# Kernel optimization log

Hardware: AMD Instinct MI355X
Metric: run time of the kernel (lower is better)

The kernel has to match this reference:

```python
import jax, jax.numpy as jnp
import numpy as np

N = 50000   # num_nodes
E = 400000  # random edges (avg degree 8)


def setup_inputs() -> dict:
    key = jax.random.key(0)
    ks = jax.random.split(key, 12)

    def w(k, shape):
        # xavier-ish scaling
        return (jax.random.normal(k, shape, jnp.float32)
                / jnp.sqrt(jnp.float32(shape[0])))

    return {
        "node_emb": jax.random.normal(ks[0], (N, 128), jnp.float32) * 0.05,
        "edge_index": jax.random.randint(ks[1], (2, E), 0, N, dtype=jnp.int32),
        "W1": w(ks[2], (128, 512)), "b1": jnp.zeros((512,), jnp.float32),
        "W2": w(ks[3], (512, 128)), "b2": jnp.zeros((128,), jnp.float32),
        "Wres": w(ks[4], (512, 128)), "bres": jnp.zeros((128,), jnp.float32),
        "Wfc1": w(ks[5], (128, 256)), "bfc1": jnp.zeros((256,), jnp.float32),
        "Wfc2": w(ks[6], (256, 1)), "bfc2": jnp.zeros((1,), jnp.float32),
    }


def reference(node_emb, edge_index, W1, b1, W2, b2, Wres, bres,
              Wfc1, bfc1, Wfc2, bfc2):
    n = node_emb.shape[0]
    loops = jnp.arange(n, dtype=edge_index.dtype)
    # explicit add_self_loops in forward + GCNConv's internal gcn_norm self
    # loops => each node gets TWO self loops (faithful to the torch code).
    src = jnp.concatenate([edge_index[0], loops, loops])
    dst = jnp.concatenate([edge_index[1], loops, loops])

    deg = jax.ops.segment_sum(jnp.ones(src.shape, node_emb.dtype), dst,
                              num_segments=n)
    dinv = jnp.where(deg > 0, jax.lax.rsqrt(deg), 0.0)
    norm = dinv[src] * dinv[dst]  # [Etot]

    def gcn(x, W, b):
        h = x @ W                                    # [N, out]
        msg = h[src] * norm[:, None]                 # gather + scale
        agg = jax.ops.segment_sum(msg, dst, num_segments=n)  # scatter-add
        return agg + b

    x1 = jax.nn.relu(gcn(node_emb, W1, b1))   # [N, 512] (dropout = eval/id)
    x2 = jax.nn.relu(gcn(x1, W2, b2))          # [N, 128]
    x = x2 + x1 @ Wres + bres                  # residual projection
    A = jax.nn.relu(x @ Wfc1 + bfc1) @ Wfc2 + bfc2  # [N, 1]
    return (x, A)
```

## Files before the change

kernel.cpp:

```cpp
#include <hip/hip_runtime.h>


typedef unsigned short u16;
typedef short bf16x8 __attribute__((ext_vector_type(8)));
typedef unsigned short us8 __attribute__((ext_vector_type(8)));
typedef float f32x4 __attribute__((ext_vector_type(4)));

static inline int cdiv_ll(long long a, long long b) { return (int)((a + b - 1) / b); }

__device__ inline float bf2f(u16 u) {
    union { unsigned int i; float f; } v; v.i = ((unsigned int)u) << 16; return v.f;
}
__device__ inline u16 f2bf(float x) {
    union { float f; unsigned int i; } v; v.f = x;
    unsigned int r = v.i + 0x7fffu + ((v.i >> 16) & 1u);
    return (u16)(r >> 16);
}


__global__ __launch_bounds__(256) void setup_kernel(const float* __restrict__ emb,
                                                    const float* __restrict__ W1,
                                                    const float* __restrict__ W2,
                                                    const float* __restrict__ Wres,
                                                    const float* __restrict__ Wfc1,
                                                    const float* __restrict__ bfc2,
                                                    u16* __restrict__ embb,
                                                    u16* __restrict__ W1t,
                                                    u16* __restrict__ Wct,
                                                    u16* __restrict__ Wfc1t,
                                                    int* __restrict__ cnt,
                                                    float* __restrict__ Aout,
                                                    int N) {
    long long r = (long long)blockIdx.x * 256 + threadIdx.x;
    const long long nf2b = (long long)N * 32;
    if (r < nf2b) {
        float4 v = ((const float4*)emb)[r];
        uint2 o;
        o.x = (unsigned)f2bf(v.x) | ((unsigned)f2bf(v.y) << 16);
        o.y = (unsigned)f2bf(v.z) | ((unsigned)f2bf(v.w) << 16);
        ((uint2*)embb)[r] = o;
        return;
    }
    r -= nf2b;
    if (r < 512 * 128) {
        int n = (int)(r / 128), k = (int)(r % 128);
        W1t[r] = f2bf(W1[(size_t)k * 512 + n]);
        return;
    }
    r -= 512 * 128;
    if (r < 256 * 512) {
        int n = (int)(r / 512), k = (int)(r % 512);
        float v = (n < 128) ? W2[(size_t)k * 128 + n] : Wres[(size_t)k * 128 + (n - 128)];
        Wct[r] = f2bf(v);
        return;
    }
    r -= 256 * 512;
    if (r < 256 * 128) {
        int n = (int)(r / 128), k = (int)(r % 128);
        Wfc1t[r] = f2bf(Wfc1[(size_t)k * 256 + n]);
        return;
    }
    r -= 256 * 128;
    if (r < N) { cnt[(int)r] = 0; return; }
    r -= N;
    if (r < N) Aout[(int)r] = bfc2[0];
}


__global__ __launch_bounds__(256) void hist_kernel(const int* __restrict__ dst,
                                                   int* __restrict__ cnt, int E) {
    int e = blockIdx.x * 256 + threadIdx.x;
    if (e < E) atomicAdd(&cnt[dst[e]], 1);
}

__global__ __launch_bounds__(256) void scanA_kernel(const int* __restrict__ cnt,
                                                    int* __restrict__ excl,
                                                    int* __restrict__ bsum, int N) {
    __shared__ int tmp[256];
    int i = blockIdx.x * 256 + threadIdx.x;
    int v = (i < N) ? cnt[i] : 0;
    tmp[threadIdx.x] = v;
    __syncthreads();
    for (int o = 1; o < 256; o <<= 1) {
        int t = (threadIdx.x >= (unsigned)o) ? tmp[threadIdx.x - o] : 0;
        __syncthreads();
        tmp[threadIdx.x] += t;
        __syncthreads();
    }
    if (i < N) excl[i] = tmp[threadIdx.x] - v;
    if (threadIdx.x == 255) bsum[blockIdx.x] = tmp[255];
}

__global__ __launch_bounds__(256) void scanC2_kernel(const int* __restrict__ excl,
                                                     const int* __restrict__ bsum,
                                                     const int* __restrict__ cnt,
                                                     int* __restrict__ rowptr,
                                                     int* __restrict__ cursor,
                                                     float* __restrict__ dinv,
                                                     int N, int E) {
    __shared__ int tmp[256];
    int t = threadIdx.x;
    tmp[t] = (t < (int)blockIdx.x) ? bsum[t] : 0;
    __syncthreads();
    for (int o = 128; o; o >>= 1) {
        if (t < o) tmp[t] += tmp[t + o];
        __syncthreads();
    }
    int pre = tmp[0];
    int i = blockIdx.x * 256 + t;
    if (i < N) {
        int r = excl[i] + pre;
        rowptr[i] = r;
        cursor[i] = r;
        dinv[i] = rsqrtf((float)cnt[i] + 2.0f);
    }
    if (i == 0) rowptr[N] = E;
}

__global__ __launch_bounds__(256) void fill_kernel(const int* __restrict__ src,
                                                   const int* __restrict__ dst,
                                                   const float* __restrict__ dinv,
                                                   int* __restrict__ cursor,
                                                   int* __restrict__ csr_src,
                                                   float* __restrict__ csr_w, int E) {
    int e = blockIdx.x * 256 + threadIdx.x;
    if (e >= E) return;
    int s = src[e], d = dst[e];
    int idx = atomicAdd(&cursor[d], 1);
    csr_src[idx] = s;
    csr_w[idx] = dinv[s] * dinv[d];
}


#define AGG_EDGE(SR, WR)                                                       \
    {                                                                          \
        unsigned int vv = hp[(size_t)(SR) * 64 + lane];                        \
        ax = fmaf(bf2f((u16)vv), (WR), ax);                                    \
        ay = fmaf(bf2f((u16)(vv >> 16)), (WR), ay);                            \
    }

__device__ inline void agg_row(const unsigned int* __restrict__ hp,
                               const int* __restrict__ rowptr,
                               const int* __restrict__ csr_src,
                               const float* __restrict__ csr_w,
                               const float* __restrict__ dinv,
                               int wid, int lane, float& ax, float& ay) {
    float dv = dinv[wid];
    unsigned int hv = hp[(size_t)wid * 64 + lane];
    float c0 = 2.0f * dv * dv;
    ax = bf2f((u16)hv) * c0;
    ay = bf2f((u16)(hv >> 16)) * c0;
    int e = rowptr[wid], e1 = rowptr[wid + 1];
    for (; e + 7 < e1; e += 8) {
        int s0 = csr_src[e + 0], s1 = csr_src[e + 1], s2 = csr_src[e + 2], s3 = csr_src[e + 3];
        int s4 = csr_src[e + 4], s5 = csr_src[e + 5], s6 = csr_src[e + 6], s7 = csr_src[e + 7];
        float w0 = csr_w[e + 0], w1 = csr_w[e + 1], w2 = csr_w[e + 2], w3 = csr_w[e + 3];
        float w4 = csr_w[e + 4], w5 = csr_w[e + 5], w6 = csr_w[e + 6], w7 = csr_w[e + 7];
        AGG_EDGE(s0, w0); AGG_EDGE(s1, w1); AGG_EDGE(s2, w2); AGG_EDGE(s3, w3);
        AGG_EDGE(s4, w4); AGG_EDGE(s5, w5); AGG_EDGE(s6, w6); AGG_EDGE(s7, w7);
    }
    if (e + 3 < e1) {
        int s0 = csr_src[e + 0], s1 = csr_src[e + 1], s2 = csr_src[e + 2], s3 = csr_src[e + 3];
        float w0 = csr_w[e + 0], w1 = csr_w[e + 1], w2 = csr_w[e + 2], w3 = csr_w[e + 3];
        AGG_EDGE(s0, w0); AGG_EDGE(s1, w1); AGG_EDGE(s2, w2); AGG_EDGE(s3, w3);
        e += 4;
    }
    for (; e < e1; ++e) {
        int s0 = csr_src[e]; float w0 = csr_w[e];
        AGG_EDGE(s0, w0);
    }
}

__global__ __launch_bounds__(256) void aggb_kernel(const u16* __restrict__ hb,
                                                   const int* __restrict__ rowptr,
                                                   const int* __restrict__ csr_src,
                                                   const float* __restrict__ csr_w,
                                                   const float* __restrict__ dinv,
                                                   u16* __restrict__ out, int N) {
    int wid  = (blockIdx.x * blockDim.x + threadIdx.x) >> 6;
    int lane = threadIdx.x & 63;
    if (wid >= N) return;
    float ax, ay;
    agg_row((const unsigned int*)hb, rowptr, csr_src, csr_w, dinv, wid, lane, ax, ay);
    ((unsigned int*)out)[(size_t)wid * 64 + lane] =
        (unsigned)f2bf(ax) | ((unsigned)f2bf(ay) << 16);
}

__global__ __launch_bounds__(256) void aggfin_kernel(const u16* __restrict__ hb,
                                                     const int* __restrict__ rowptr,
                                                     const int* __restrict__ csr_src,
                                                     const float* __restrict__ csr_w,
                                                     const float* __restrict__ dinv,
                                                     const float* __restrict__ b2,
                                                     const float* __restrict__ bres,
                                                     float* __restrict__ xout, int N) {
    int wid  = (blockIdx.x * blockDim.x + threadIdx.x) >> 6;
    int lane = threadIdx.x & 63;
    if (wid >= N) return;
    float ax, ay;
    agg_row((const unsigned int*)hb, rowptr, csr_src, csr_w, dinv, wid, lane, ax, ay);
    float2 bb = ((const float2*)b2)[lane];
    float2 rr = ((const float2*)bres)[lane];
    float2 hres = ((float2*)xout)[(size_t)wid * 64 + lane];
    float ox = fmaxf(ax + bb.x, 0.f) + hres.x + rr.x;
    float oy = fmaxf(ay + bb.y, 0.f) + hres.y + rr.y;
    ((float2*)xout)[(size_t)wid * 64 + lane] = make_float2(ox, oy);
}


__global__ __launch_bounds__(512) void mgemm12(const u16* __restrict__ aggE,
                                               const u16* __restrict__ W1t,
                                               const u16* __restrict__ Wct,
                                               const float* __restrict__ b1,
                                               int M,
                                               u16* __restrict__ h2b,
                                               float* __restrict__ xout) {
    extern __shared__ u16 smem[];
    u16* Ag  = smem;
    u16* Ws  = Ag + 128 * 136;
    u16* X1s = Ws + 256 * 136;
    const int LD = 136;

    const int t = threadIdx.x;
    const int bm = blockIdx.x * 128;
    const int w = t >> 6, lane = t & 63;
    const int wm = w >> 2, wn = w & 3;
    const int l15 = lane & 15, lg = lane >> 4;
    const int srow = t >> 4, scol = (t & 15) * 8;

#pragma unroll
    for (int i = 0; i < 4; ++i) {
        int row = srow + 32 * i;
        us8 v = (us8)(u16)0;
        if (bm + row < M) v = *(const us8*)(aggE + (size_t)(bm + row) * 128 + scol);
        *(us8*)&Ag[row * LD + scol] = v;
    }

    f32x4 acc2[4][4];
#pragma unroll
    for (int i = 0; i < 4; ++i)
#pragma unroll
        for (int j = 0; j < 4; ++j) acc2[i][j] = (f32x4)(0.0f);

    us8 rw1[4], rwc[8];
#pragma unroll
    for (int i = 0; i < 4; ++i)
        rw1[i] = *(const us8*)(W1t + (size_t)(srow + 32 * i) * 128 + scol);

    for (int p = 0; p < 4; ++p) {
        __syncthreads();
#pragma unroll
        for (int i = 0; i < 4; ++i)
            *(us8*)&Ws[(srow + 32 * i) * LD + scol] = rw1[i];
        __syncthreads();

#pragma unroll
        for (int i = 0; i < 8; ++i)
            rwc[i] = *(const us8*)(Wct + (size_t)(srow + 32 * i) * 512 + 128 * p + scol);

        f32x4 acc1[4][2];
#pragma unroll
        for (int i = 0; i < 4; ++i)
#pragma unroll
            for (int j = 0; j < 2; ++j) acc1[i][j] = (f32x4)(0.0f);
#pragma unroll
        for (int ks = 0; ks < 4; ++ks) {
            const int ko = 32 * ks + lg * 8;
            bf16x8 wfr[2], afr[4];
#pragma unroll
            for (int fn = 0; fn < 2; ++fn)
                wfr[fn] = *(const bf16x8*)&Ws[(32 * wn + 16 * fn + l15) * LD + ko];
#pragma unroll
            for (int fm = 0; fm < 4; ++fm)
                afr[fm] = *(const bf16x8*)&Ag[(64 * wm + 16 * fm + l15) * LD + ko];
#pragma unroll
            for (int fm = 0; fm < 4; ++fm)
#pragma unroll
                for (int fn = 0; fn < 2; ++fn)
                    acc1[fm][fn] = __builtin_amdgcn_mfma_f32_16x16x32_bf16(
                        wfr[fn], afr[fm], acc1[fm][fn], 0, 0, 0);
        }
        __syncthreads();

#pragma unroll
        for (int fm = 0; fm < 4; ++fm) {
#pragma unroll
            for (int fn = 0; fn < 2; ++fn) {
                int col1 = 32 * wn + 16 * fn + 4 * lg;
                float4 b4 = *(const float4*)&b1[128 * p + col1];
                f32x4 v = acc1[fm][fn];
                float v0 = fmaxf(v[0] + b4.x, 0.f), v1 = fmaxf(v[1] + b4.y, 0.f);
                float v2 = fmaxf(v[2] + b4.z, 0.f), v3 = fmaxf(v[3] + b4.w, 0.f);
                uint2 o;
                o.x = (unsigned)f2bf(v0) | ((unsigned)f2bf(v1) << 16);
                o.y = (unsigned)f2bf(v2) | ((unsigned)f2bf(v3) << 16);
                *(uint2*)&X1s[(64 * wm + 16 * fm + l15) * LD + col1] = o;
            }
        }
#pragma unroll
        for (int i = 0; i < 8; ++i)
            *(us8*)&Ws[(srow + 32 * i) * LD + scol] = rwc[i];
        if (p < 3) {
#pragma unroll
            for (int i = 0; i < 4; ++i)
                rw1[i] = *(const us8*)(W1t + (size_t)(128 * (p + 1) + srow + 32 * i) * 128 + scol);
        }
        __syncthreads();

#pragma unroll
        for (int ks = 0; ks < 4; ++ks) {
            const int ko = 32 * ks + lg * 8;
            bf16x8 wfr[4], xfr[4];
#pragma unroll
            for (int fn = 0; fn < 4; ++fn)
                wfr[fn] = *(const bf16x8*)&Ws[(64 * wn + 16 * fn + l15) * LD + ko];
#pragma unroll
            for (int fm = 0; fm < 4; ++fm)
                xfr[fm] = *(const bf16x8*)&X1s[(64 * wm + 16 * fm + l15) * LD + ko];
#pragma unroll
            for (int fm = 0; fm < 4; ++fm)
#pragma unroll
                for (int fn = 0; fn < 4; ++fn)
                    acc2[fm][fn] = __builtin_amdgcn_mfma_f32_16x16x32_bf16(
                        wfr[fn], xfr[fm], acc2[fm][fn], 0, 0, 0);
        }
    }

#pragma unroll
    for (int fm = 0; fm < 4; ++fm) {
        const int row = bm + 64 * wm + 16 * fm + l15;
        if (row >= M) continue;
#pragma unroll
        for (int fn = 0; fn < 4; ++fn) {
            const int col = 64 * wn + 16 * fn + 4 * lg;
            f32x4 v = acc2[fm][fn];
            if (col < 128) {
                uint2 o;
                o.x = (unsigned)f2bf(v[0]) | ((unsigned)f2bf(v[1]) << 16);
                o.y = (unsigned)f2bf(v[2]) | ((unsigned)f2bf(v[3]) << 16);
                *(uint2*)(h2b + (size_t)row * 128 + col) = o;
            } else {
                *(float4*)(xout + (size_t)row * 128 + (col - 128)) =
                    make_float4(v[0], v[1], v[2], v[3]);
            }
        }
    }
}


__global__ __launch_bounds__(512) void head_gemm(const float* __restrict__ X,
                                                 const u16* __restrict__ Bt,
                                                 int M,
                                                 const float* __restrict__ bias,
                                                 const float* __restrict__ w2,
                                                 float* __restrict__ Cf) {
    __shared__ u16 As[128][72];
    __shared__ u16 Bs[256][72];
    const int t = threadIdx.x;
    const int bm = blockIdx.x * 128;
    const int w = t >> 6, lane = t & 63;
    const int wm = w >> 2, wn = w & 3;
    const int l15 = lane & 15, lg = lane >> 4;
    const int srow = t >> 3, scol = (t & 7) * 8;
    const int K = 128;

    f32x4 acc[4][4];
#pragma unroll
    for (int i = 0; i < 4; ++i)
#pragma unroll
        for (int j = 0; j < 4; ++j) acc[i][j] = (f32x4)(0.0f);

    for (int kk = 0; kk < K; kk += 64) {
#pragma unroll
        for (int i = 0; i < 2; ++i) {
            int row = srow + 64 * i;
            uint4 o = make_uint4(0u, 0u, 0u, 0u);
            if (bm + row < M) {
                const float* src = X + (size_t)(bm + row) * K + kk + scol;
                float4 a = *(const float4*)src;
                float4 b = *(const float4*)(src + 4);
                o.x = (unsigned)f2bf(a.x) | ((unsigned)f2bf(a.y) << 16);
                o.y = (unsigned)f2bf(a.z) | ((unsigned)f2bf(a.w) << 16);
                o.z = (unsigned)f2bf(b.x) | ((unsigned)f2bf(b.y) << 16);
                o.w = (unsigned)f2bf(b.z) | ((unsigned)f2bf(b.w) << 16);
            }
            *(uint4*)&As[row][scol] = o;
        }
#pragma unroll
        for (int i = 0; i < 4; ++i) {
            int row = srow + 64 * i;
            *(us8*)&Bs[row][scol] =
                *(const us8*)(Bt + (size_t)row * K + kk + scol);
        }
        __syncthreads();
#pragma unroll
        for (int ks = 0; ks < 2; ++ks) {
            const int ko = 32 * ks + lg * 8;
            bf16x8 bfr[4], afr[4];
#pragma unroll
            for (int fn = 0; fn < 4; ++fn)
                bfr[fn] = *(const bf16x8*)&Bs[64 * wn + 16 * fn + l15][ko];
#pragma unroll
            for (int fm = 0; fm < 4; ++fm)
                afr[fm] = *(const bf16x8*)&As[64 * wm + 16 * fm + l15][ko];
#pragma unroll
            for (int fm = 0; fm < 4; ++fm)
#pragma unroll
                for (int fn = 0; fn < 4; ++fn)
                    acc[fm][fn] = __builtin_amdgcn_mfma_f32_16x16x32_bf16(
                        bfr[fn], afr[fm], acc[fm][fn], 0, 0, 0);
        }
        __syncthreads();
    }

    float4 bl4[4], wl4[4];
#pragma unroll
    for (int fn = 0; fn < 4; ++fn) {
        int c = 64 * wn + 16 * fn + 4 * lg;
        bl4[fn] = *(const float4*)&bias[c];
        wl4[fn] = *(const float4*)&w2[c];
    }
#pragma unroll
    for (int fm = 0; fm < 4; ++fm) {
        float p = 0.f;
#pragma unroll
        for (int fn = 0; fn < 4; ++fn) {
            p += fmaxf(acc[fm][fn][0] + bl4[fn].x, 0.f) * wl4[fn].x;
            p += fmaxf(acc[fm][fn][1] + bl4[fn].y, 0.f) * wl4[fn].y;
            p += fmaxf(acc[fm][fn][2] + bl4[fn].z, 0.f) * wl4[fn].z;
            p += fmaxf(acc[fm][fn][3] + bl4[fn].w, 0.f) * wl4[fn].w;
        }
        p += __shfl_xor(p, 16);
        p += __shfl_xor(p, 32);
        int row = bm + 64 * wm + 16 * fm + l15;
        if (lane < 16 && row < M) atomicAdd(&Cf[row], p);
    }
}


extern "C" void kernel_launch(void* const* d_in, const int* in_sizes, int n_in,
                              void* d_out, int out_size, void* d_ws, size_t ws_size,
                              hipStream_t stream) {
    const float* emb  = (const float*)d_in[0];
    const int*   eidx = (const int*)d_in[1];
    const float* W1   = (const float*)d_in[2];
    const float* b1   = (const float*)d_in[3];
    const float* W2   = (const float*)d_in[4];
    const float* b2   = (const float*)d_in[5];
    const float* Wres = (const float*)d_in[6];
    const float* bres = (const float*)d_in[7];
    const float* Wfc1 = (const float*)d_in[8];
    const float* bfc1 = (const float*)d_in[9];
    const float* Wfc2 = (const float*)d_in[10];
    const float* bfc2 = (const float*)d_in[11];

    const int N = in_sizes[0] / 128;
    const int E = in_sizes[1] / 2;
    const int* srcv = eidx;
    const int* dstv = eidx + E;

    float* out  = (float*)d_out;
    float* xout = out;
    float* Aout = out + (size_t)N * 128;

    char* p = (char*)d_ws;
    float* dinv  = (float*)p;            p += (size_t)N * 4;
    float* csr_w = (float*)p;            p += (size_t)E * 4;
    u16*  embb   = (u16*)p;              p += (size_t)N * 128 * 2;
    u16*  aggEb  = (u16*)p;              p += (size_t)N * 128 * 2;
    u16*  h2b    = (u16*)p;              p += (size_t)N * 128 * 2;
    u16*  W1t    = (u16*)p;              p += (size_t)512 * 128 * 2;
    u16*  Wct    = (u16*)p;              p += (size_t)256 * 512 * 2;
    u16*  Wfc1t  = (u16*)p;              p += (size_t)256 * 128 * 2;
    int*  cnt     = (int*)p;             p += (size_t)N * 4;
    int*  excl    = (int*)p;             p += (size_t)N * 4;
    int*  rowptr  = (int*)p;             p += (size_t)(N + 1) * 4;
    int*  cursor  = (int*)p;             p += (size_t)N * 4;
    int*  bsum    = (int*)p;             p += 256 * 4;
    int*  csr_src = (int*)p;             p += (size_t)E * 4;

    const int T  = 256;
    const int nb = cdiv_ll(N, 256);

    const long long setup_work = (long long)N * 32 + 512 * 128 + 256 * 512
                               + 256 * 128 + (long long)N + (long long)N;
    setup_kernel<<<cdiv_ll(setup_work, T), T, 0, stream>>>(
        emb, W1, W2, Wres, Wfc1, bfc2, embb, W1t, Wct, Wfc1t, cnt, Aout, N);

    hist_kernel<<<cdiv_ll(E, T), T, 0, stream>>>(dstv, cnt, E);
    scanA_kernel<<<nb, T, 0, stream>>>(cnt, excl, bsum, N);
    scanC2_kernel<<<nb, T, 0, stream>>>(excl, bsum, cnt, rowptr, cursor, dinv, N, E);
    fill_kernel<<<cdiv_ll(E, T), T, 0, stream>>>(srcv, dstv, dinv, cursor, csr_src, csr_w, E);

    aggb_kernel<<<cdiv_ll((long long)N * 64, T), T, 0, stream>>>(
        embb, rowptr, csr_src, csr_w, dinv, aggEb, N);

    const size_t lds12 = (size_t)(128 * 136 + 256 * 136 + 128 * 136) * sizeof(u16);
    mgemm12<<<cdiv_ll(N, 128), 512, lds12, stream>>>(
        aggEb, W1t, Wct, b1, N, h2b, xout);

    aggfin_kernel<<<cdiv_ll((long long)N * 64, T), T, 0, stream>>>(
        h2b, rowptr, csr_src, csr_w, dinv, b2, bres, xout, N);

    head_gemm<<<cdiv_ll(N, 128), 512, 0, stream>>>(
        xout, Wfc1t, N, bfc1, Wfc2, Aout);
}
```

Before: 175.0 us.

## Split wavefront into four edge groups with 16-byte gathers in aggregation

The two sparse aggregation kernels are merged into one templated kernel. Each wavefront now splits its 64 lanes into four groups of 16. Each group processes every fourth edge and each lane gathers 8 bf16 values (16 bytes) per edge instead of 2. The partial sums are combined with cross-lane shuffles, and a single group writes the result. This is meant to put more independent row gathers in flight per wavefront and to use wider loads, at the cost of extra shuffle reductions and idle lanes in the epilogue.

```diff
diff --git a/kernel.cpp b/kernel.cpp
--- a/kernel.cpp
+++ b/kernel.cpp
@@ -15,6 +15,9 @@
     union { float f; unsigned int i; } v; v.f = x;
     unsigned int r = v.i + 0x7fffu + ((v.i >> 16) & 1u);
     return (u16)(r >> 16);
+}
+__device__ inline unsigned pk2(float a, float b) {
+    return (unsigned)f2bf(a) | ((unsigned)f2bf(b) << 16);
 }
 
 
@@ -36,8 +39,8 @@
     if (r < nf2b) {
         float4 v = ((const float4*)emb)[r];
         uint2 o;
-        o.x = (unsigned)f2bf(v.x) | ((unsigned)f2bf(v.y) << 16);
-        o.y = (unsigned)f2bf(v.z) | ((unsigned)f2bf(v.w) << 16);
+        o.x = pk2(v.x, v.y);
+        o.y = pk2(v.z, v.w);
         ((uint2*)embb)[r] = o;
         return;
     }
@@ -132,79 +135,95 @@
 }
 
 
-#define AGG_EDGE(SR, WR)                                                       \
+#define FMA8(VV, W)                                                            \
     {                                                                          \
-        unsigned int vv = hp[(size_t)(SR) * 64 + lane];                        \
-        ax = fmaf(bf2f((u16)vv), (WR), ax);                                    \
-        ay = fmaf(bf2f((u16)(vv >> 16)), (WR), ay);                            \
-    }
-
-__device__ inline void agg_row(const unsigned int* __restrict__ hp,
-                               const int* __restrict__ rowptr,
-                               const int* __restrict__ csr_src,
-                               const float* __restrict__ csr_w,
-                               const float* __restrict__ dinv,
-                               int wid, int lane, float& ax, float& ay) {
-    float dv = dinv[wid];
-    unsigned int hv = hp[(size_t)wid * 64 + lane];
-    float c0 = 2.0f * dv * dv;
-    ax = bf2f((u16)hv) * c0;
-    ay = bf2f((u16)(hv >> 16)) * c0;
-    int e = rowptr[wid], e1 = rowptr[wid + 1];
-    for (; e + 7 < e1; e += 8) {
-        int s0 = csr_src[e + 0], s1 = csr_src[e + 1], s2 = csr_src[e + 2], s3 = csr_src[e + 3];
-        int s4 = csr_src[e + 4], s5 = csr_src[e + 5], s6 = csr_src[e + 6], s7 = csr_src[e + 7];
-        float w0 = csr_w[e + 0], w1 = csr_w[e + 1], w2 = csr_w[e + 2], w3 = csr_w[e + 3];
-        float w4 = csr_w[e + 4], w5 = csr_w[e + 5], w6 = csr_w[e + 6], w7 = csr_w[e + 7];
-        AGG_EDGE(s0, w0); AGG_EDGE(s1, w1); AGG_EDGE(s2, w2); AGG_EDGE(s3, w3);
-        AGG_EDGE(s4, w4); AGG_EDGE(s5, w5); AGG_EDGE(s6, w6); AGG_EDGE(s7, w7);
-    }
-    if (e + 3 < e1) {
-        int s0 = csr_src[e + 0], s1 = csr_src[e + 1], s2 = csr_src[e + 2], s3 = csr_src[e + 3];
-        float w0 = csr_w[e + 0], w1 = csr_w[e + 1], w2 = csr_w[e + 2], w3 = csr_w[e + 3];
-        AGG_EDGE(s0, w0); AGG_EDGE(s1, w1); AGG_EDGE(s2, w2); AGG_EDGE(s3, w3);
-        e += 4;
-    }
-    for (; e < e1; ++e) {
-        int s0 = csr_src[e]; float w0 = csr_w[e];
-        AGG_EDGE(s0, w0);
-    }
-}
-
-__global__ __launch_bounds__(256) void aggb_kernel(const u16* __restrict__ hb,
+        acc0 = fmaf(bf2f((u16)(VV).x), (W), acc0);                             \
+        acc1 = fmaf(bf2f((u16)((VV).x >> 16)), (W), acc1);                     \
+        acc2 = fmaf(bf2f((u16)(VV).y), (W), acc2);                             \
+        acc3 = fmaf(bf2f((u16)((VV).y >> 16)), (W), acc3);                     \
+        acc4 = fmaf(bf2f((u16)(VV).z), (W), acc4);                             \
+        acc5 = fmaf(bf2f((u16)((VV).z >> 16)), (W), acc5);                     \
+        acc6 = fmaf(bf2f((u16)(VV).w), (W), acc6);                             \
+        acc7 = fmaf(bf2f((u16)((VV).w >> 16)), (W), acc7);                     \
+    }
+
+template <int FINAL>
+__global__ __launch_bounds__(256) void aggq_kernel(const u16* __restrict__ hb,
                                                    const int* __restrict__ rowptr,
                                                    const int* __restrict__ csr_src,
                                                    const float* __restrict__ csr_w,
                                                    const float* __restrict__ dinv,
-                                                   u16* __restrict__ out, int N) {
+                                                   const float* __restrict__ b2,
+                                                   const float* __restrict__ bres,
+                                                   float* __restrict__ xout,
+                                                   u16* __restrict__ outb, int N) {
     int wid  = (blockIdx.x * blockDim.x + threadIdx.x) >> 6;
     int lane = threadIdx.x & 63;
+    int g = lane >> 4, l = lane & 15;
     if (wid >= N) return;
-    float ax, ay;
-    agg_row((const unsigned int*)hb, rowptr, csr_src, csr_w, dinv, wid, lane, ax, ay);
-    ((unsigned int*)out)[(size_t)wid * 64 + lane] =
-        (unsigned)f2bf(ax) | ((unsigned)f2bf(ay) << 16);
-}
-
-__global__ __launch_bounds__(256) void aggfin_kernel(const u16* __restrict__ hb,
-                                                     const int* __restrict__ rowptr,
-                                                     const int* __restrict__ csr_src,
-                                                     const float* __restrict__ csr_w,
-                                                     const float* __restrict__ dinv,
-                                                     const float* __restrict__ b2,
-                                                     const float* __restrict__ bres,
-                                                     float* __restrict__ xout, int N) {
-    int wid  = (blockIdx.x * blockDim.x + threadIdx.x) >> 6;
-    int lane = threadIdx.x & 63;
-    if (wid >= N) return;
-    float ax, ay;
-    agg_row((const unsigned int*)hb, rowptr, csr_src, csr_w, dinv, wid, lane, ax, ay);
-    float2 bb = ((const float2*)b2)[lane];
-    float2 rr = ((const float2*)bres)[lane];
-    float2 hres = ((float2*)xout)[(size_t)wid * 64 + lane];
-    float ox = fmaxf(ax + bb.x, 0.f) + hres.x + rr.x;
-    float oy = fmaxf(ay + bb.y, 0.f) + hres.y + rr.y;
-    ((float2*)xout)[(size_t)wid * 64 + lane] = make_float2(ox, oy);
+    const uint4* hp4 = (const uint4*)hb;
+
+    float acc0 = 0.f, acc1 = 0.f, acc2 = 0.f, acc3 = 0.f;
+    float acc4 = 0.f, acc5 = 0.f, acc6 = 0.f, acc7 = 0.f;
+    float dv = dinv[wid];
+    if (g == 0) {
+        uint4 hv = hp4[(size_t)wid * 16 + l];
+        float c0 = 2.0f * dv * dv;
+        FMA8(hv, c0);
+    }
+
+    int e  = rowptr[wid] + g;
+    int e1 = rowptr[wid + 1];
+    for (; e + 4 < e1; e += 8) {
+        int   s0 = csr_src[e],     s1 = csr_src[e + 4];
+        float w0 = csr_w[e],       w1 = csr_w[e + 4];
+        uint4 v0 = hp4[(size_t)s0 * 16 + l];
+        uint4 v1 = hp4[(size_t)s1 * 16 + l];
+        FMA8(v0, w0);
+        FMA8(v1, w1);
+    }
+    if (e < e1) {
+        int s0 = csr_src[e]; float w0 = csr_w[e];
+        uint4 v0 = hp4[(size_t)s0 * 16 + l];
+        FMA8(v0, w0);
+    }
+
+    acc0 += __shfl_xor(acc0, 16); acc0 += __shfl_xor(acc0, 32);
+    acc1 += __shfl_xor(acc1, 16); acc1 += __shfl_xor(acc1, 32);
+    acc2 += __shfl_xor(acc2, 16); acc2 += __shfl_xor(acc2, 32);
+    acc3 += __shfl_xor(acc3, 16); acc3 += __shfl_xor(acc3, 32);
+    acc4 += __shfl_xor(acc4, 16); acc4 += __shfl_xor(acc4, 32);
+    acc5 += __shfl_xor(acc5, 16); acc5 += __shfl_xor(acc5, 32);
+    acc6 += __shfl_xor(acc6, 16); acc6 += __shfl_xor(acc6, 32);
+    acc7 += __shfl_xor(acc7, 16); acc7 += __shfl_xor(acc7, 32);
+
+    if (g != 0) return;
+    if (FINAL) {
+        const float* b2p = b2 + 8 * l;
+        const float* brp = bres + 8 * l;
+        float* xp = xout + (size_t)wid * 128 + 8 * l;
+        float4 bb0 = *(const float4*)b2p,  bb1 = *(const float4*)(b2p + 4);
+        float4 br0 = *(const float4*)brp,  br1 = *(const float4*)(brp + 4);
+        float4 h0  = *(const float4*)xp,   h1  = *(const float4*)(xp + 4);
+        float4 o0, o1;
+        o0.x = fmaxf(acc0 + bb0.x, 0.f) + h0.x + br0.x;
+        o0.y = fmaxf(acc1 + bb0.y, 0.f) + h0.y + br0.y;
+        o0.z = fmaxf(acc2 + bb0.z, 0.f) + h0.z + br0.z;
+        o0.w = fmaxf(acc3 + bb0.w, 0.f) + h0.w + br0.w;
+        o1.x = fmaxf(acc4 + bb1.x, 0.f) + h1.x + br1.x;
+        o1.y = fmaxf(acc5 + bb1.y, 0.f) + h1.y + br1.y;
+        o1.z = fmaxf(acc6 + bb1.z, 0.f) + h1.z + br1.z;
+        o1.w = fmaxf(acc7 + bb1.w, 0.f) + h1.w + br1.w;
+        *(float4*)xp = o0;
+        *(float4*)(xp + 4) = o1;
+    } else {
+        uint4 o;
+        o.x = pk2(acc0, acc1);
+        o.y = pk2(acc2, acc3);
+        o.z = pk2(acc4, acc5);
+        o.w = pk2(acc6, acc7);
+        ((uint4*)outb)[(size_t)wid * 16 + l] = o;
+    }
 }
 
 
@@ -292,8 +311,8 @@
                 float v0 = fmaxf(v[0] + b4.x, 0.f), v1 = fmaxf(v[1] + b4.y, 0.f);
                 float v2 = fmaxf(v[2] + b4.z, 0.f), v3 = fmaxf(v[3] + b4.w, 0.f);
                 uint2 o;
-                o.x = (unsigned)f2bf(v0) | ((unsigned)f2bf(v1) << 16);
-                o.y = (unsigned)f2bf(v2) | ((unsigned)f2bf(v3) << 16);
+                o.x = pk2(v0, v1);
+                o.y = pk2(v2, v3);
                 *(uint2*)&X1s[(64 * wm + 16 * fm + l15) * LD + col1] = o;
             }
         }
@@ -336,8 +355,8 @@
             f32x4 v = acc2[fm][fn];
             if (col < 128) {
                 uint2 o;
-                o.x = (unsigned)f2bf(v[0]) | ((unsigned)f2bf(v[1]) << 16);
-                o.y = (unsigned)f2bf(v[2]) | ((unsigned)f2bf(v[3]) << 16);
+                o.x = pk2(v[0], v[1]);
+                o.y = pk2(v[2], v[3]);
                 *(uint2*)(h2b + (size_t)row * 128 + col) = o;
             } else {
                 *(float4*)(xout + (size_t)row * 128 + (col - 128)) =
@@ -379,10 +398,10 @@
                 const float* src = X + (size_t)(bm + row) * K + kk + scol;
                 float4 a = *(const float4*)src;
                 float4 b = *(const float4*)(src + 4);
-                o.x = (unsigned)f2bf(a.x) | ((unsigned)f2bf(a.y) << 16);
-                o.y = (unsigned)f2bf(a.z) | ((unsigned)f2bf(a.w) << 16);
-                o.z = (unsigned)f2bf(b.x) | ((unsigned)f2bf(b.y) << 16);
-                o.w = (unsigned)f2bf(b.z) | ((unsigned)f2bf(b.w) << 16);
+                o.x = pk2(a.x, a.y);
+                o.y = pk2(a.z, a.w);
+                o.z = pk2(b.x, b.y);
+                o.w = pk2(b.z, b.w);
             }
             *(uint4*)&As[row][scol] = o;
         }
@@ -492,15 +511,15 @@
     scanC2_kernel<<<nb, T, 0, stream>>>(excl, bsum, cnt, rowptr, cursor, dinv, N, E);
     fill_kernel<<<cdiv_ll(E, T), T, 0, stream>>>(srcv, dstv, dinv, cursor, csr_src, csr_w, E);
 
-    aggb_kernel<<<cdiv_ll((long long)N * 64, T), T, 0, stream>>>(
-        embb, rowptr, csr_src, csr_w, dinv, aggEb, N);
+    aggq_kernel<0><<<cdiv_ll((long long)N * 64, T), T, 0, stream>>>(
+        embb, rowptr, csr_src, csr_w, dinv, nullptr, nullptr, nullptr, aggEb, N);
 
     const size_t lds12 = (size_t)(128 * 136 + 256 * 136 + 128 * 136) * sizeof(u16);
     mgemm12<<<cdiv_ll(N, 128), 512, lds12, stream>>>(
         aggEb, W1t, Wct, b1, N, h2b, xout);
 
-    aggfin_kernel<<<cdiv_ll((long long)N * 64, T), T, 0, stream>>>(
-        h2b, rowptr, csr_src, csr_w, dinv, b2, bres, xout, N);
+    aggq_kernel<1><<<cdiv_ll((long long)N * 64, T), T, 0, stream>>>(
+        h2b, rowptr, csr_src, csr_w, dinv, b2, bres, xout, nullptr, N);
 
     head_gemm<<<cdiv_ll(N, 128), 512, 0, stream>>>(
         xout, Wfc1t, N, bfc1, Wfc2, Aout);
```

Measured after the change: 179.5 us. 2.6% more time.
